# Optimization experiments

Hardware: AMD Instinct MI355X
Metric: run time of the kernel (lower is better)

The kernel has to match this reference:

```python
import jax, jax.numpy as jnp
import numpy as np

VOXEL_SIZE = np.array([0.32, 0.32, 6.0], dtype=np.float32)
SPATIAL_SIZE = np.array([-74.88, 74.88, -74.88, 74.88, -3.0, 3.0], dtype=np.float32)
# voxel_spatial_size = ceil((max-min)/voxel_size) per dim -> [468, 468, 1]
GRID = np.array([int(np.ceil((SPATIAL_SIZE[2*i+1]-SPATIAL_SIZE[2*i])/VOXEL_SIZE[i])) for i in range(3)], dtype=np.int32)
# voxel origin = floor(min / voxel_size) -> [-234, -234, -1]
ORIGIN = np.floor(SPATIAL_SIZE[0::2] / VOXEL_SIZE).astype(np.int32)
VOL = int(np.prod(GRID))  # 468*468*1
# row-major id multipliers: prods[1:]+[1] -> [468, 1, 1]
SHIFT = np.array([int(np.prod(GRID[1:])), int(np.prod(GRID[2:])), 1], dtype=np.int32)
VOXEL_FEATURE_MIN = -1000.0

B, N, D_IN, MLP = 4, 100000, 16, 128


def setup_inputs() -> dict:
    key = jax.random.key(0)
    k1, k2, k3, k4, k5 = jax.random.split(key, 5)
    xy = jax.random.uniform(k1, (B, N, 2), minval=-80.0, maxval=80.0)
    z = jax.random.uniform(k2, (B, N, 1), minval=-4.0, maxval=4.0)
    point_xyz = jnp.concatenate([xy, z], axis=-1)
    point_feature = jax.random.normal(k3, (B, N, D_IN), dtype=jnp.float32)
    point_mask = jax.random.uniform(k4, (B, N)) < 0.95
    W = jax.random.normal(k5, (D_IN + 3, MLP), dtype=jnp.float32) * 0.1
    b = jnp.zeros((MLP,), dtype=jnp.float32)
    return {"point_xyz": point_xyz, "point_feature": point_feature,
            "point_mask": point_mask, "W": W, "b": b}


def reference(point_xyz, point_feature, point_mask, W, b):
    vs = jnp.asarray(VOXEL_SIZE, dtype=point_xyz.dtype)
    # PointToVoxel
    pvx_f = jnp.floor(point_xyz / vs)                      # [B,N,3] float voxel coords
    point_voxel_feature = point_xyz - pvx_f * vs           # delta within voxel
    pvx = pvx_f.astype(jnp.int32) - jnp.asarray(ORIGIN)    # shifted int voxel coords
    grid = jnp.asarray(GRID)
    in_bounds = jnp.all((pvx >= 0) & (pvx < grid), axis=-1)
    voxel_mask = in_bounds & point_mask                    # [B,N]
    vid = jnp.sum(pvx * jnp.asarray(SHIFT), axis=-1)       # [B,N]
    vid = vid + jnp.arange(B, dtype=jnp.int32)[:, None] * VOL
    vid = vid * voxel_mask.astype(jnp.int32)               # invalid -> 0
    # point net (Dense + ReLU) on [point_feature, voxel delta]
    feat = jnp.concatenate([point_feature, point_voxel_feature], axis=-1)
    mf = voxel_mask.astype(feat.dtype)[..., None]
    feat = feat * mf
    feat = jax.nn.relu(jnp.einsum('bnd,dk->bnk', feat, W) + b)
    feat = feat * mf
    # scatter-max into dense voxel grid
    seg = jax.ops.segment_max(feat.reshape(-1, MLP), vid.reshape(-1),
                              num_segments=B * VOL)
    seg = jnp.where(seg > VOXEL_FEATURE_MIN, seg, 0.0)
    # z dim is 1 -> squeezed: [B, 468, 468, MLP]
    return seg.reshape(B, int(GRID[0]), int(GRID[1]), MLP)
```

## Files before the change

kernel.cpp:

```cpp
#include <hip/hip_runtime.h>
#include <hip/hip_bf16.h>
#include <stdint.h>

#define BB   4
#define NN   100000
#define TOTAL (BB * NN)
#define DIN  16
#define DF   19
#define KO   128
#define GX   468
#define GY   468
#define VOL  (GX * GY)
#define NV   (BB * VOL)
#define CAP  12
#define SLOT_F 20
#define NWAVES (NV / 64)

typedef float vfloat2 __attribute__((ext_vector_type(2)));

#define WS_COUNTS   0
#define WS_FLAG     (NV)
#define WS_PACKED   (NV + 16)

__global__ __launch_bounds__(256) void prep(
    int4* __restrict__ counts4,
    const uint4* __restrict__ mask_words,
    int* __restrict__ flag)
{
    if (blockIdx.x == 0) {
        __shared__ int sA, sB;
        if (threadIdx.x == 0) { sA = 0; sB = 0; }
        __syncthreads();
        int a = 0, b = 0;
        #pragma unroll
        for (int it = 0; it < 4; ++it) {
            uint4 w = mask_words[it * 256 + threadIdx.x];
            unsigned lo = (w.x & 0xFFu) | (w.y & 0xFFu) | (w.z & 0xFFu) | (w.w & 0xFFu);
            unsigned hi = (w.x & 0xFFFFFF00u) | (w.y & 0xFFFFFF00u) |
                          (w.z & 0xFFFFFF00u) | (w.w & 0xFFFFFF00u);
            if (hi) a = 1;
            if (lo) b = 1;
        }
        if (a) atomicOr(&sA, 1);
        if (b) atomicOr(&sB, 1);
        __syncthreads();
        if (threadIdx.x == 0) flag[0] = (sA && sB) ? 1 : 4;
    }
    const int i = blockIdx.x * 256 + threadIdx.x;
    if (i < NV / 4) counts4[i] = make_int4(0, 0, 0, 0);
}

__global__ __launch_bounds__(256) void pass1_bin(
    const float* __restrict__ xyz,
    const float* __restrict__ pfeat,
    const unsigned char* __restrict__ mask_raw,
    const int* __restrict__ flag,
    int* __restrict__ counts,
    float* __restrict__ packed)
{
    const int p = blockIdx.x * 256 + threadIdx.x;
    if (p >= TOTAL) return;
    const float x = xyz[p * 3 + 0];
    const float y = xyz[p * 3 + 1];
    const float z = xyz[p * 3 + 2];
    bool m;
    if (flag[0] == 4) m = (((const int*)mask_raw)[p] != 0);
    else              m = (mask_raw[p] != 0);
    const float fx = floorf(x / 0.32f);
    const float fy = floorf(y / 0.32f);
    const float fz = floorf(z / 6.0f);
    const int ix = (int)fx + 234;
    const int iy = (int)fy + 234;
    const int iz = (int)fz + 1;
    const bool inb = ((unsigned)ix < (unsigned)GX) &
                     ((unsigned)iy < (unsigned)GY) &
                     (iz == 0) & m;
    if (!inb) return;
    const int vid = (p / NN) * VOL + ix * GY + iy;
    const int rank = atomicAdd(&counts[vid], 1);
    if (rank >= CAP) return;

    float4* slot = (float4*)(packed + (size_t)(vid * CAP + rank) * SLOT_F);
    const float4* pf4 = (const float4*)(pfeat + (size_t)p * DIN);
    slot[0] = pf4[0];
    slot[1] = pf4[1];
    slot[2] = pf4[2];
    slot[3] = pf4[3];
    slot[4] = make_float4(x - fx * 0.32f, y - fy * 0.32f, z - fz * 6.0f, 0.f);
}

__global__ __launch_bounds__(256) void fused_write(
    const float* __restrict__ W,
    const float* __restrict__ bias,
    const int* __restrict__ counts,
    const float* __restrict__ packed,
    float* __restrict__ out)
{
    const int lane = threadIdx.x & 63;
    const int wid  = (blockIdx.x * 256 + threadIdx.x) >> 6;
    if (wid >= NWAVES) return;
    const int v0 = wid * 64;

    const int c_mine = counts[v0 + lane];
    const unsigned long long occ = __ballot(c_mine > 0);

    const float2* W2 = (const float2*)W;
    float2 w[DF];
    #pragma unroll
    for (int d = 0; d < DF; ++d) w[d] = W2[d * 64 + lane];
    const float2 bb = ((const float2*)bias)[lane];

    vfloat2* dst0 = (vfloat2*)(out + (size_t)v0 * KO) + lane;

    {
        vfloat2 zz = {0.f, 0.f};
        unsigned long long emp = ~occ;
        while (emp) {
            const int j = __builtin_ctzll(emp);
            emp &= emp - 1;
            __builtin_nontemporal_store(zz, dst0 + (size_t)j * 64);
        }
    }

    unsigned long long rem = occ;
    int j_cur = -1;
    float4 q0, q1, q2, q3, q4;
    if (rem) {
        j_cur = __builtin_ctzll(rem);
        rem &= rem - 1;
        const float4* base = (const float4*)(packed +
                             (size_t)(v0 + j_cur) * CAP * SLOT_F);
        q0 = base[0]; q1 = base[1]; q2 = base[2]; q3 = base[3]; q4 = base[4];
    }
    while (j_cur >= 0) {
        int j_nxt = -1;
        float4 n0, n1, n2, n3, n4;
        if (rem) {
            j_nxt = __builtin_ctzll(rem);
            rem &= rem - 1;
            const float4* nb = (const float4*)(packed +
                               (size_t)(v0 + j_nxt) * CAP * SLOT_F);
            n0 = nb[0]; n1 = nb[1]; n2 = nb[2]; n3 = nb[3]; n4 = nb[4];
        }

        const int c = min(__shfl(c_mine, j_cur), CAP);
        const float4* base = (const float4*)(packed +
                             (size_t)(v0 + j_cur) * CAP * SLOT_F);
        float m0 = -3.0e38f, m1 = -3.0e38f;
        for (int t = 0; t < c; ++t) {
            float4 p0, p1, p2, p3, p4;
            if (t == 0) { p0 = q0; p1 = q1; p2 = q2; p3 = q3; p4 = q4; }
            else {
                p0 = base[t * 5 + 0]; p1 = base[t * 5 + 1];
                p2 = base[t * 5 + 2]; p3 = base[t * 5 + 3];
                p4 = base[t * 5 + 4];
            }
            float a0 = bb.x, a1 = bb.y;
            a0 = fmaf(p0.x, w[0].x, a0);  a1 = fmaf(p0.x, w[0].y, a1);
            a0 = fmaf(p0.y, w[1].x, a0);  a1 = fmaf(p0.y, w[1].y, a1);
            a0 = fmaf(p0.z, w[2].x, a0);  a1 = fmaf(p0.z, w[2].y, a1);
            a0 = fmaf(p0.w, w[3].x, a0);  a1 = fmaf(p0.w, w[3].y, a1);
            a0 = fmaf(p1.x, w[4].x, a0);  a1 = fmaf(p1.x, w[4].y, a1);
            a0 = fmaf(p1.y, w[5].x, a0);  a1 = fmaf(p1.y, w[5].y, a1);
            a0 = fmaf(p1.z, w[6].x, a0);  a1 = fmaf(p1.z, w[6].y, a1);
            a0 = fmaf(p1.w, w[7].x, a0);  a1 = fmaf(p1.w, w[7].y, a1);
            a0 = fmaf(p2.x, w[8].x, a0);  a1 = fmaf(p2.x, w[8].y, a1);
            a0 = fmaf(p2.y, w[9].x, a0);  a1 = fmaf(p2.y, w[9].y, a1);
            a0 = fmaf(p2.z, w[10].x, a0); a1 = fmaf(p2.z, w[10].y, a1);
            a0 = fmaf(p2.w, w[11].x, a0); a1 = fmaf(p2.w, w[11].y, a1);
            a0 = fmaf(p3.x, w[12].x, a0); a1 = fmaf(p3.x, w[12].y, a1);
            a0 = fmaf(p3.y, w[13].x, a0); a1 = fmaf(p3.y, w[13].y, a1);
            a0 = fmaf(p3.z, w[14].x, a0); a1 = fmaf(p3.z, w[14].y, a1);
            a0 = fmaf(p3.w, w[15].x, a0); a1 = fmaf(p3.w, w[15].y, a1);
            a0 = fmaf(p4.x, w[16].x, a0); a1 = fmaf(p4.x, w[16].y, a1);
            a0 = fmaf(p4.y, w[17].x, a0); a1 = fmaf(p4.y, w[17].y, a1);
            a0 = fmaf(p4.z, w[18].x, a0); a1 = fmaf(p4.z, w[18].y, a1);
            m0 = fmaxf(m0, a0);
            m1 = fmaxf(m1, a1);
        }
        vfloat2 rv = {fmaxf(m0, 0.f), fmaxf(m1, 0.f)};
        __builtin_nontemporal_store(rv, dst0 + (size_t)j_cur * 64);

        j_cur = j_nxt;
        q0 = n0; q1 = n1; q2 = n2; q3 = n3; q4 = n4;
    }
}

extern "C" void kernel_launch(void* const* d_in, const int* in_sizes, int n_in,
                              void* d_out, int out_size, void* d_ws, size_t ws_size,
                              hipStream_t stream) {
    const float* xyz   = (const float*)d_in[0];
    const float* pfeat = (const float*)d_in[1];
    const unsigned char* mask = (const unsigned char*)d_in[2];
    const float* W     = (const float*)d_in[3];
    const float* bias  = (const float*)d_in[4];
    float* out = (float*)d_out;
    int* ws = (int*)d_ws;

    int*   counts = ws + WS_COUNTS;
    int*   flag   = ws + WS_FLAG;
    float* packed = (float*)(ws + WS_PACKED);

    prep<<<(NV / 4 + 255) / 256, 256, 0, stream>>>((int4*)counts,
                                                   (const uint4*)mask, flag);
    pass1_bin<<<(TOTAL + 255) / 256, 256, 0, stream>>>(xyz, pfeat, mask, flag,
                                                       counts, packed);
    fused_write<<<(NWAVES + 3) / 4, 256, 0, stream>>>(W, bias, counts,
                                                      packed, out);
}
```

Before: 536.4 us.

## Replace bin-and-gather with per-point MLP and global atomicMax scatter

```diff
diff --git a/kernel.cpp b/kernel.cpp
--- a/kernel.cpp
+++ b/kernel.cpp
@@ -1,5 +1,4 @@
 #include <hip/hip_runtime.h>
-#include <hip/hip_bf16.h>
 #include <stdint.h>
 
 #define BB   4
@@ -12,18 +11,14 @@
 #define GY   468
 #define VOL  (GX * GY)
 #define NV   (BB * VOL)
-#define CAP  12
-#define SLOT_F 20
-#define NWAVES (NV / 64)
+#define OUT_F4 ((size_t)NV * KO / 4)
 
-typedef float vfloat2 __attribute__((ext_vector_type(2)));
+typedef float vfloat4 __attribute__((ext_vector_type(4)));
 
-#define WS_COUNTS   0
-#define WS_FLAG     (NV)
-#define WS_PACKED   (NV + 16)
+#define WS_FLAG 0
 
-__global__ __launch_bounds__(256) void prep(
-    int4* __restrict__ counts4,
+__global__ __launch_bounds__(256) void fill_zero(
+    vfloat4* __restrict__ out4,
     const uint4* __restrict__ mask_words,
     int* __restrict__ flag)
 {
@@ -46,143 +41,98 @@
         __syncthreads();
         if (threadIdx.x == 0) flag[0] = (sA && sB) ? 1 : 4;
     }
-    const int i = blockIdx.x * 256 + threadIdx.x;
-    if (i < NV / 4) counts4[i] = make_int4(0, 0, 0, 0);
+    const vfloat4 z = {0.f, 0.f, 0.f, 0.f};
+    const size_t stride = (size_t)gridDim.x * 256;
+    for (size_t i = (size_t)blockIdx.x * 256 + threadIdx.x; i < OUT_F4; i += stride)
+        __builtin_nontemporal_store(z, out4 + i);
 }
 
-__global__ __launch_bounds__(256) void pass1_bin(
+__global__ __launch_bounds__(256) void points(
     const float* __restrict__ xyz,
     const float* __restrict__ pfeat,
     const unsigned char* __restrict__ mask_raw,
     const int* __restrict__ flag,
-    int* __restrict__ counts,
-    float* __restrict__ packed)
+    const float* __restrict__ W,
+    const float* __restrict__ bias,
+    float* __restrict__ out)
 {
+    __shared__ float sW[DF * KO];
+    __shared__ float sB[KO];
+    for (int i = threadIdx.x; i < DF * KO; i += 256) sW[i] = W[i];
+    if (threadIdx.x < KO) sB[threadIdx.x] = bias[threadIdx.x];
+
     const int p = blockIdx.x * 256 + threadIdx.x;
+    float x = 0.f, y = 0.f, z = 0.f;
+    bool m = false;
+    float4 pf0, pf1, pf2, pf3;
+    pf0 = pf1 = pf2 = pf3 = make_float4(0.f, 0.f, 0.f, 0.f);
+    if (p < TOTAL) {
+        x = xyz[p * 3 + 0];
+        y = xyz[p * 3 + 1];
+        z = xyz[p * 3 + 2];
+        if (flag[0] == 4) m = (((const int*)mask_raw)[p] != 0);
+        else              m = (mask_raw[p] != 0);
+        const float4* pf4 = (const float4*)(pfeat + (size_t)p * DIN);
+        pf0 = pf4[0]; pf1 = pf4[1]; pf2 = pf4[2]; pf3 = pf4[3];
+    }
+    __syncthreads();
     if (p >= TOTAL) return;
-    const float x = xyz[p * 3 + 0];
-    const float y = xyz[p * 3 + 1];
-    const float z = xyz[p * 3 + 2];
-    bool m;
-    if (flag[0] == 4) m = (((const int*)mask_raw)[p] != 0);
-    else              m = (mask_raw[p] != 0);
+
     const float fx = floorf(x / 0.32f);
     const float fy = floorf(y / 0.32f);
     const float fz = floorf(z / 6.0f);
     const int ix = (int)fx + 234;
     const int iy = (int)fy + 234;
     const int iz = (int)fz + 1;
-    const bool inb = ((unsigned)ix < (unsigned)GX) &
-                     ((unsigned)iy < (unsigned)GY) &
-                     (iz == 0) & m;
-    if (!inb) return;
-    const int vid = (p / NN) * VOL + ix * GY + iy;
-    const int rank = atomicAdd(&counts[vid], 1);
-    if (rank >= CAP) return;
+    const bool valid = ((unsigned)ix < (unsigned)GX) &
+                       ((unsigned)iy < (unsigned)GY) &
+                       (iz == 0) & m;
+    if (__ballot(valid) == 0ULL) return;
 
-    float4* slot = (float4*)(packed + (size_t)(vid * CAP + rank) * SLOT_F);
-    const float4* pf4 = (const float4*)(pfeat + (size_t)p * DIN);
-    slot[0] = pf4[0];
-    slot[1] = pf4[1];
-    slot[2] = pf4[2];
-    slot[3] = pf4[3];
-    slot[4] = make_float4(x - fx * 0.32f, y - fy * 0.32f, z - fz * 6.0f, 0.f);
-}
+    float f[DF];
+    f[0]  = pf0.x; f[1]  = pf0.y; f[2]  = pf0.z; f[3]  = pf0.w;
+    f[4]  = pf1.x; f[5]  = pf1.y; f[6]  = pf1.z; f[7]  = pf1.w;
+    f[8]  = pf2.x; f[9]  = pf2.y; f[10] = pf2.z; f[11] = pf2.w;
+    f[12] = pf3.x; f[13] = pf3.y; f[14] = pf3.z; f[15] = pf3.w;
+    f[16] = x - fx * 0.32f;
+    f[17] = y - fy * 0.32f;
+    f[18] = z - fz * 6.0f;
 
-__global__ __launch_bounds__(256) void fused_write(
-    const float* __restrict__ W,
-    const float* __restrict__ bias,
-    const int* __restrict__ counts,
-    const float* __restrict__ packed,
-    float* __restrict__ out)
-{
-    const int lane = threadIdx.x & 63;
-    const int wid  = (blockIdx.x * 256 + threadIdx.x) >> 6;
-    if (wid >= NWAVES) return;
-    const int v0 = wid * 64;
+    const int vid = valid ? ((p / NN) * VOL + ix * GY + iy) : 0;
+    int* row = (int*)out + (size_t)vid * KO;
 
-    const int c_mine = counts[v0 + lane];
-    const unsigned long long occ = __ballot(c_mine > 0);
-
-    const float2* W2 = (const float2*)W;
-    float2 w[DF];
     #pragma unroll
-    for (int d = 0; d < DF; ++d) w[d] = W2[d * 64 + lane];
-    const float2 bb = ((const float2*)bias)[lane];
-
-    vfloat2* dst0 = (vfloat2*)(out + (size_t)v0 * KO) + lane;
-
-    {
-        vfloat2 zz = {0.f, 0.f};
-        unsigned long long emp = ~occ;
-        while (emp) {
-            const int j = __builtin_ctzll(emp);
-            emp &= emp - 1;
-            __builtin_nontemporal_store(zz, dst0 + (size_t)j * 64);
+    for (int c = 0; c < 8; ++c) {
+        float acc[16];
+        {
+            const float4* b4 = (const float4*)(sB + c * 16);
+            #pragma unroll
+            for (int q = 0; q < 4; ++q) {
+                float4 bv = b4[q];
+                acc[q * 4 + 0] = bv.x; acc[q * 4 + 1] = bv.y;
+                acc[q * 4 + 2] = bv.z; acc[q * 4 + 3] = bv.w;
+            }
         }
-    }
-
-    unsigned long long rem = occ;
-    int j_cur = -1;
-    float4 q0, q1, q2, q3, q4;
-    if (rem) {
-        j_cur = __builtin_ctzll(rem);
-        rem &= rem - 1;
-        const float4* base = (const float4*)(packed +
-                             (size_t)(v0 + j_cur) * CAP * SLOT_F);
-        q0 = base[0]; q1 = base[1]; q2 = base[2]; q3 = base[3]; q4 = base[4];
-    }
-    while (j_cur >= 0) {
-        int j_nxt = -1;
-        float4 n0, n1, n2, n3, n4;
-        if (rem) {
-            j_nxt = __builtin_ctzll(rem);
-            rem &= rem - 1;
-            const float4* nb = (const float4*)(packed +
-                               (size_t)(v0 + j_nxt) * CAP * SLOT_F);
-            n0 = nb[0]; n1 = nb[1]; n2 = nb[2]; n3 = nb[3]; n4 = nb[4];
+        #pragma unroll
+        for (int d = 0; d < DF; ++d) {
+            const float fd = f[d];
+            const float4* wq = (const float4*)(sW + d * KO + c * 16);
+            #pragma unroll
+            for (int q = 0; q < 4; ++q) {
+                float4 wv = wq[q];
+                acc[q * 4 + 0] = fmaf(fd, wv.x, acc[q * 4 + 0]);
+                acc[q * 4 + 1] = fmaf(fd, wv.y, acc[q * 4 + 1]);
+                acc[q * 4 + 2] = fmaf(fd, wv.z, acc[q * 4 + 2]);
+                acc[q * 4 + 3] = fmaf(fd, wv.w, acc[q * 4 + 3]);
+            }
         }
-
-        const int c = min(__shfl(c_mine, j_cur), CAP);
-        const float4* base = (const float4*)(packed +
-                             (size_t)(v0 + j_cur) * CAP * SLOT_F);
-        float m0 = -3.0e38f, m1 = -3.0e38f;
-        for (int t = 0; t < c; ++t) {
-            float4 p0, p1, p2, p3, p4;
-            if (t == 0) { p0 = q0; p1 = q1; p2 = q2; p3 = q3; p4 = q4; }
-            else {
-                p0 = base[t * 5 + 0]; p1 = base[t * 5 + 1];
-                p2 = base[t * 5 + 2]; p3 = base[t * 5 + 3];
-                p4 = base[t * 5 + 4];
+        if (valid) {
+            #pragma unroll
+            for (int j = 0; j < 16; ++j) {
+                const float r = fmaxf(acc[j], 0.f);
+                atomicMax(row + c * 16 + j, __float_as_int(r));
             }
-            float a0 = bb.x, a1 = bb.y;
-            a0 = fmaf(p0.x, w[0].x, a0);  a1 = fmaf(p0.x, w[0].y, a1);
-            a0 = fmaf(p0.y, w[1].x, a0);  a1 = fmaf(p0.y, w[1].y, a1);
-            a0 = fmaf(p0.z, w[2].x, a0);  a1 = fmaf(p0.z, w[2].y, a1);
-            a0 = fmaf(p0.w, w[3].x, a0);  a1 = fmaf(p0.w, w[3].y, a1);
-            a0 = fmaf(p1.x, w[4].x, a0);  a1 = fmaf(p1.x, w[4].y, a1);
-            a0 = fmaf(p1.y, w[5].x, a0);  a1 = fmaf(p1.y, w[5].y, a1);
-            a0 = fmaf(p1.z, w[6].x, a0);  a1 = fmaf(p1.z, w[6].y, a1);
-            a0 = fmaf(p1.w, w[7].x, a0);  a1 = fmaf(p1.w, w[7].y, a1);
-            a0 = fmaf(p2.x, w[8].x, a0);  a1 = fmaf(p2.x, w[8].y, a1);
-            a0 = fmaf(p2.y, w[9].x, a0);  a1 = fmaf(p2.y, w[9].y, a1);
-            a0 = fmaf(p2.z, w[10].x, a0); a1 = fmaf(p2.z, w[10].y, a1);
-            a0 = fmaf(p2.w, w[11].x, a0); a1 = fmaf(p2.w, w[11].y, a1);
-            a0 = fmaf(p3.x, w[12].x, a0); a1 = fmaf(p3.x, w[12].y, a1);
-            a0 = fmaf(p3.y, w[13].x, a0); a1 = fmaf(p3.y, w[13].y, a1);
-            a0 = fmaf(p3.z, w[14].x, a0); a1 = fmaf(p3.z, w[14].y, a1);
-            a0 = fmaf(p3.w, w[15].x, a0); a1 = fmaf(p3.w, w[15].y, a1);
-            a0 = fmaf(p4.x, w[16].x, a0); a1 = fmaf(p4.x, w[16].y, a1);
-            a0 = fmaf(p4.y, w[17].x, a0); a1 = fmaf(p4.y, w[17].y, a1);
-            a0 = fmaf(p4.z, w[18].x, a0); a1 = fmaf(p4.z, w[18].y, a1);
-            m0 = fmaxf(m0, a0);
-            m1 = fmaxf(m1, a1);
         }
-        vfloat2 rv = {fmaxf(m0, 0.f), fmaxf(m1, 0.f)};
-        __builtin_nontemporal_store(rv, dst0 + (size_t)j_cur * 64);
-
-        j_cur = j_nxt;
-        q0 = n0; q1 = n1; q2 = n2; q3 = n3; q4 = n4;
     }
 }
 
@@ -195,16 +145,9 @@
     const float* W     = (const float*)d_in[3];
     const float* bias  = (const float*)d_in[4];
     float* out = (float*)d_out;
-    int* ws = (int*)d_ws;
+    int* flag = (int*)d_ws + WS_FLAG;
 
-    int*   counts = ws + WS_COUNTS;
-    int*   flag   = ws + WS_FLAG;
-    float* packed = (float*)(ws + WS_PACKED);
-
-    prep<<<(NV / 4 + 255) / 256, 256, 0, stream>>>((int4*)counts,
-                                                   (const uint4*)mask, flag);
-    pass1_bin<<<(TOTAL + 255) / 256, 256, 0, stream>>>(xyz, pfeat, mask, flag,
-                                                       counts, packed);
-    fused_write<<<(NWAVES + 3) / 4, 256, 0, stream>>>(W, bias, counts,
-                                                      packed, out);
+    fill_zero<<<2048, 256, 0, stream>>>((vfloat4*)out, (const uint4*)mask, flag);
+    points<<<(TOTAL + 255) / 256, 256, 0, stream>>>(xyz, pfeat, mask, flag,
+                                                    W, bias, out);
 }
```

New measurement: 1.383 ms. 158% more time.

## Overlap dense output zero-fill with point binning and skip empty waves

Applied to the files above, without the earlier changes.

```diff
diff --git a/kernel.cpp b/kernel.cpp
--- a/kernel.cpp
+++ b/kernel.cpp
@@ -1,5 +1,4 @@
 #include <hip/hip_runtime.h>
-#include <hip/hip_bf16.h>
 #include <stdint.h>
 
 #define BB   4
@@ -15,8 +14,13 @@
 #define CAP  12
 #define SLOT_F 20
 #define NWAVES (NV / 64)
+#define OUT_F4 ((size_t)NV * KO / 4)
+
+#define FILLB 6144
+#define BINB  2048
 
 typedef float vfloat2 __attribute__((ext_vector_type(2)));
+typedef float vfloat4 __attribute__((ext_vector_type(4)));
 
 #define WS_COUNTS   0
 #define WS_FLAG     (NV)
@@ -50,7 +54,8 @@
     if (i < NV / 4) counts4[i] = make_int4(0, 0, 0, 0);
 }
 
-__global__ __launch_bounds__(256) void pass1_bin(
+__global__ __launch_bounds__(256) void fill_and_bin(
+    vfloat4* __restrict__ out4,
     const float* __restrict__ xyz,
     const float* __restrict__ pfeat,
     const unsigned char* __restrict__ mask_raw,
@@ -58,7 +63,16 @@
     int* __restrict__ counts,
     float* __restrict__ packed)
 {
-    const int p = blockIdx.x * 256 + threadIdx.x;
+    const int r = blockIdx.x & 3;
+    if (r != 3) {
+        const size_t fid = (size_t)(blockIdx.x >> 2) * 3 + r;
+        const vfloat4 z = {0.f, 0.f, 0.f, 0.f};
+        const size_t stride = (size_t)FILLB * 256;
+        for (size_t i = fid * 256 + threadIdx.x; i < OUT_F4; i += stride)
+            __builtin_nontemporal_store(z, out4 + i);
+        return;
+    }
+    const int p = (blockIdx.x >> 2) * 256 + threadIdx.x;
     if (p >= TOTAL) return;
     const float x = xyz[p * 3 + 0];
     const float y = xyz[p * 3 + 1];
@@ -89,7 +103,7 @@
     slot[4] = make_float4(x - fx * 0.32f, y - fy * 0.32f, z - fz * 6.0f, 0.f);
 }
 
-__global__ __launch_bounds__(256) void fused_write(
+__global__ __launch_bounds__(256) void write_occ(
     const float* __restrict__ W,
     const float* __restrict__ bias,
     const int* __restrict__ counts,
@@ -103,6 +117,7 @@
 
     const int c_mine = counts[v0 + lane];
     const unsigned long long occ = __ballot(c_mine > 0);
+    if (!occ) return;
 
     const float2* W2 = (const float2*)W;
     float2 w[DF];
@@ -112,22 +127,11 @@
 
     vfloat2* dst0 = (vfloat2*)(out + (size_t)v0 * KO) + lane;
 
+    unsigned long long rem = occ;
+    int j_cur = __builtin_ctzll(rem);
+    rem &= rem - 1;
+    float4 q0, q1, q2, q3, q4;
     {
-        vfloat2 zz = {0.f, 0.f};
-        unsigned long long emp = ~occ;
-        while (emp) {
-            const int j = __builtin_ctzll(emp);
-            emp &= emp - 1;
-            __builtin_nontemporal_store(zz, dst0 + (size_t)j * 64);
-        }
-    }
-
-    unsigned long long rem = occ;
-    int j_cur = -1;
-    float4 q0, q1, q2, q3, q4;
-    if (rem) {
-        j_cur = __builtin_ctzll(rem);
-        rem &= rem - 1;
         const float4* base = (const float4*)(packed +
                              (size_t)(v0 + j_cur) * CAP * SLOT_F);
         q0 = base[0]; q1 = base[1]; q2 = base[2]; q3 = base[3]; q4 = base[4];
@@ -203,8 +207,8 @@
 
     prep<<<(NV / 4 + 255) / 256, 256, 0, stream>>>((int4*)counts,
                                                    (const uint4*)mask, flag);
-    pass1_bin<<<(TOTAL + 255) / 256, 256, 0, stream>>>(xyz, pfeat, mask, flag,
-                                                       counts, packed);
-    fused_write<<<(NWAVES + 3) / 4, 256, 0, stream>>>(W, bias, counts,
-                                                      packed, out);
-}
+    fill_and_bin<<<FILLB + BINB, 256, 0, stream>>>((vfloat4*)out, xyz, pfeat,
+                                                   mask, flag, counts, packed);
+    write_occ<<<(NWAVES + 3) / 4, 256, 0, stream>>>(W, bias, counts,
+                                                    packed, out);
+}
```

After: 556.6 us. +3.8%, slower.

## Fuse prep, binning and write kernels into one cooperative persistent kernel

Applied to the files above, without the earlier changes.

```diff
diff --git a/kernel.cpp b/kernel.cpp
--- a/kernel.cpp
+++ b/kernel.cpp
@@ -1,6 +1,8 @@
 #include <hip/hip_runtime.h>
-#include <hip/hip_bf16.h>
+#include <hip/hip_cooperative_groups.h>
 #include <stdint.h>
+
+namespace cg = cooperative_groups;
 
 #define BB   4
 #define NN   100000
@@ -22,87 +24,21 @@
 #define WS_FLAG     (NV)
 #define WS_PACKED   (NV + 16)
 
-__global__ __launch_bounds__(256) void prep(
-    int4* __restrict__ counts4,
-    const uint4* __restrict__ mask_words,
-    int* __restrict__ flag)
-{
-    if (blockIdx.x == 0) {
-        __shared__ int sA, sB;
-        if (threadIdx.x == 0) { sA = 0; sB = 0; }
-        __syncthreads();
-        int a = 0, b = 0;
-        #pragma unroll
-        for (int it = 0; it < 4; ++it) {
-            uint4 w = mask_words[it * 256 + threadIdx.x];
-            unsigned lo = (w.x & 0xFFu) | (w.y & 0xFFu) | (w.z & 0xFFu) | (w.w & 0xFFu);
-            unsigned hi = (w.x & 0xFFFFFF00u) | (w.y & 0xFFFFFF00u) |
-                          (w.z & 0xFFFFFF00u) | (w.w & 0xFFFFFF00u);
-            if (hi) a = 1;
-            if (lo) b = 1;
-        }
-        if (a) atomicOr(&sA, 1);
-        if (b) atomicOr(&sB, 1);
-        __syncthreads();
-        if (threadIdx.x == 0) flag[0] = (sA && sB) ? 1 : 4;
-    }
-    const int i = blockIdx.x * 256 + threadIdx.x;
-    if (i < NV / 4) counts4[i] = make_int4(0, 0, 0, 0);
-}
-
-__global__ __launch_bounds__(256) void pass1_bin(
+__global__ __launch_bounds__(256, 4) void mega(
     const float* __restrict__ xyz,
     const float* __restrict__ pfeat,
     const unsigned char* __restrict__ mask_raw,
-    const int* __restrict__ flag,
-    int* __restrict__ counts,
-    float* __restrict__ packed)
-{
-    const int p = blockIdx.x * 256 + threadIdx.x;
-    if (p >= TOTAL) return;
-    const float x = xyz[p * 3 + 0];
-    const float y = xyz[p * 3 + 1];
-    const float z = xyz[p * 3 + 2];
-    bool m;
-    if (flag[0] == 4) m = (((const int*)mask_raw)[p] != 0);
-    else              m = (mask_raw[p] != 0);
-    const float fx = floorf(x / 0.32f);
-    const float fy = floorf(y / 0.32f);
-    const float fz = floorf(z / 6.0f);
-    const int ix = (int)fx + 234;
-    const int iy = (int)fy + 234;
-    const int iz = (int)fz + 1;
-    const bool inb = ((unsigned)ix < (unsigned)GX) &
-                     ((unsigned)iy < (unsigned)GY) &
-                     (iz == 0) & m;
-    if (!inb) return;
-    const int vid = (p / NN) * VOL + ix * GY + iy;
-    const int rank = atomicAdd(&counts[vid], 1);
-    if (rank >= CAP) return;
-
-    float4* slot = (float4*)(packed + (size_t)(vid * CAP + rank) * SLOT_F);
-    const float4* pf4 = (const float4*)(pfeat + (size_t)p * DIN);
-    slot[0] = pf4[0];
-    slot[1] = pf4[1];
-    slot[2] = pf4[2];
-    slot[3] = pf4[3];
-    slot[4] = make_float4(x - fx * 0.32f, y - fy * 0.32f, z - fz * 6.0f, 0.f);
-}
-
-__global__ __launch_bounds__(256) void fused_write(
     const float* __restrict__ W,
     const float* __restrict__ bias,
-    const int* __restrict__ counts,
-    const float* __restrict__ packed,
+    int* __restrict__ counts,
+    int* __restrict__ flag,
+    float* __restrict__ packed,
     float* __restrict__ out)
 {
+    cg::grid_group grid = cg::this_grid();
+    const int tid  = blockIdx.x * 256 + threadIdx.x;
+    const int nth  = gridDim.x * 256;
     const int lane = threadIdx.x & 63;
-    const int wid  = (blockIdx.x * 256 + threadIdx.x) >> 6;
-    if (wid >= NWAVES) return;
-    const int v0 = wid * 64;
-
-    const int c_mine = counts[v0 + lane];
-    const unsigned long long occ = __ballot(c_mine > 0);
 
     const float2* W2 = (const float2*)W;
     float2 w[DF];
@@ -110,79 +46,148 @@
     for (int d = 0; d < DF; ++d) w[d] = W2[d * 64 + lane];
     const float2 bb = ((const float2*)bias)[lane];
 
-    vfloat2* dst0 = (vfloat2*)(out + (size_t)v0 * KO) + lane;
-
+    if (blockIdx.x == 0) {
+        __shared__ int sA, sB;
+        if (threadIdx.x == 0) { sA = 0; sB = 0; }
+        __syncthreads();
+        const uint4* mask_words = (const uint4*)mask_raw;
+        int a = 0, b = 0;
+        #pragma unroll
+        for (int it = 0; it < 4; ++it) {
+            uint4 mw = mask_words[it * 256 + threadIdx.x];
+            unsigned lo = (mw.x & 0xFFu) | (mw.y & 0xFFu) | (mw.z & 0xFFu) | (mw.w & 0xFFu);
+            unsigned hi = (mw.x & 0xFFFFFF00u) | (mw.y & 0xFFFFFF00u) |
+                          (mw.z & 0xFFFFFF00u) | (mw.w & 0xFFFFFF00u);
+            if (hi) a = 1;
+            if (lo) b = 1;
+        }
+        if (a) atomicOr(&sA, 1);
+        if (b) atomicOr(&sB, 1);
+        __syncthreads();
+        if (threadIdx.x == 0) flag[0] = (sA && sB) ? 1 : 4;
+    }
     {
-        vfloat2 zz = {0.f, 0.f};
-        unsigned long long emp = ~occ;
-        while (emp) {
-            const int j = __builtin_ctzll(emp);
-            emp &= emp - 1;
-            __builtin_nontemporal_store(zz, dst0 + (size_t)j * 64);
-        }
-    }
-
-    unsigned long long rem = occ;
-    int j_cur = -1;
-    float4 q0, q1, q2, q3, q4;
-    if (rem) {
-        j_cur = __builtin_ctzll(rem);
-        rem &= rem - 1;
-        const float4* base = (const float4*)(packed +
-                             (size_t)(v0 + j_cur) * CAP * SLOT_F);
-        q0 = base[0]; q1 = base[1]; q2 = base[2]; q3 = base[3]; q4 = base[4];
-    }
-    while (j_cur >= 0) {
-        int j_nxt = -1;
-        float4 n0, n1, n2, n3, n4;
+        int4* counts4 = (int4*)counts;
+        for (int i = tid; i < NV / 4; i += nth)
+            counts4[i] = make_int4(0, 0, 0, 0);
+    }
+    grid.sync();
+
+    {
+        const int mflag = flag[0];
+        for (int p = tid; p < TOTAL; p += nth) {
+            const float x = xyz[p * 3 + 0];
+            const float y = xyz[p * 3 + 1];
+            const float z = xyz[p * 3 + 2];
+            bool m;
+            if (mflag == 4) m = (((const int*)mask_raw)[p] != 0);
+            else            m = (mask_raw[p] != 0);
+            const float fx = floorf(x / 0.32f);
+            const float fy = floorf(y / 0.32f);
+            const float fz = floorf(z / 6.0f);
+            const int ix = (int)fx + 234;
+            const int iy = (int)fy + 234;
+            const int iz = (int)fz + 1;
+            const bool inb = ((unsigned)ix < (unsigned)GX) &
+                             ((unsigned)iy < (unsigned)GY) &
+                             (iz == 0) & m;
+            if (!inb) continue;
+            const int vid = (p / NN) * VOL + ix * GY + iy;
+            const int rank = atomicAdd(&counts[vid], 1);
+            if (rank >= CAP) continue;
+
+            float4* slot = (float4*)(packed + (size_t)(vid * CAP + rank) * SLOT_F);
+            const float4* pf4 = (const float4*)(pfeat + (size_t)p * DIN);
+            slot[0] = pf4[0];
+            slot[1] = pf4[1];
+            slot[2] = pf4[2];
+            slot[3] = pf4[3];
+            slot[4] = make_float4(x - fx * 0.32f, y - fy * 0.32f, z - fz * 6.0f, 0.f);
+        }
+    }
+    grid.sync();
+
+    const int nwav = nth >> 6;
+    for (int wid = tid >> 6; wid < NWAVES; wid += nwav) {
+        const int v0 = wid * 64;
+
+        const int c_mine = counts[v0 + lane];
+        const unsigned long long occ = __ballot(c_mine > 0);
+
+        vfloat2* dst0 = (vfloat2*)(out + (size_t)v0 * KO) + lane;
+
+        {
+            vfloat2 zz = {0.f, 0.f};
+            unsigned long long emp = ~occ;
+            while (emp) {
+                const int j = __builtin_ctzll(emp);
+                emp &= emp - 1;
+                __builtin_nontemporal_store(zz, dst0 + (size_t)j * 64);
+            }
+        }
+
+        unsigned long long rem = occ;
+        int j_cur = -1;
+        float4 q0, q1, q2, q3, q4;
         if (rem) {
-            j_nxt = __builtin_ctzll(rem);
+            j_cur = __builtin_ctzll(rem);
             rem &= rem - 1;
-            const float4* nb = (const float4*)(packed +
-                               (size_t)(v0 + j_nxt) * CAP * SLOT_F);
-            n0 = nb[0]; n1 = nb[1]; n2 = nb[2]; n3 = nb[3]; n4 = nb[4];
-        }
-
-        const int c = min(__shfl(c_mine, j_cur), CAP);
-        const float4* base = (const float4*)(packed +
-                             (size_t)(v0 + j_cur) * CAP * SLOT_F);
-        float m0 = -3.0e38f, m1 = -3.0e38f;
-        for (int t = 0; t < c; ++t) {
-            float4 p0, p1, p2, p3, p4;
-            if (t == 0) { p0 = q0; p1 = q1; p2 = q2; p3 = q3; p4 = q4; }
-            else {
-                p0 = base[t * 5 + 0]; p1 = base[t * 5 + 1];
-                p2 = base[t * 5 + 2]; p3 = base[t * 5 + 3];
-                p4 = base[t * 5 + 4];
+            const float4* base = (const float4*)(packed +
+                                 (size_t)(v0 + j_cur) * CAP * SLOT_F);
+            q0 = base[0]; q1 = base[1]; q2 = base[2]; q3 = base[3]; q4 = base[4];
+        }
+        while (j_cur >= 0) {
+            int j_nxt = -1;
+            float4 n0, n1, n2, n3, n4;
+            if (rem) {
+                j_nxt = __builtin_ctzll(rem);
+                rem &= rem - 1;
+                const float4* nb = (const float4*)(packed +
+                                   (size_t)(v0 + j_nxt) * CAP * SLOT_F);
+                n0 = nb[0]; n1 = nb[1]; n2 = nb[2]; n3 = nb[3]; n4 = nb[4];
             }
-            float a0 = bb.x, a1 = bb.y;
-            a0 = fmaf(p0.x, w[0].x, a0);  a1 = fmaf(p0.x, w[0].y, a1);
-            a0 = fmaf(p0.y, w[1].x, a0);  a1 = fmaf(p0.y, w[1].y, a1);
-            a0 = fmaf(p0.z, w[2].x, a0);  a1 = fmaf(p0.z, w[2].y, a1);
-            a0 = fmaf(p0.w, w[3].x, a0);  a1 = fmaf(p0.w, w[3].y, a1);
-            a0 = fmaf(p1.x, w[4].x, a0);  a1 = fmaf(p1.x, w[4].y, a1);
-            a0 = fmaf(p1.y, w[5].x, a0);  a1 = fmaf(p1.y, w[5].y, a1);
-            a0 = fmaf(p1.z, w[6].x, a0);  a1 = fmaf(p1.z, w[6].y, a1);
-            a0 = fmaf(p1.w, w[7].x, a0);  a1 = fmaf(p1.w, w[7].y, a1);
-            a0 = fmaf(p2.x, w[8].x, a0);  a1 = fmaf(p2.x, w[8].y, a1);
-            a0 = fmaf(p2.y, w[9].x, a0);  a1 = fmaf(p2.y, w[9].y, a1);
-            a0 = fmaf(p2.z, w[10].x, a0); a1 = fmaf(p2.z, w[10].y, a1);
-            a0 = fmaf(p2.w, w[11].x, a0); a1 = fmaf(p2.w, w[11].y, a1);
-            a0 = fmaf(p3.x, w[12].x, a0); a1 = fmaf(p3.x, w[12].y, a1);
-            a0 = fmaf(p3.y, w[13].x, a0); a1 = fmaf(p3.y, w[13].y, a1);
-            a0 = fmaf(p3.z, w[14].x, a0); a1 = fmaf(p3.z, w[14].y, a1);
-            a0 = fmaf(p3.w, w[15].x, a0); a1 = fmaf(p3.w, w[15].y, a1);
-            a0 = fmaf(p4.x, w[16].x, a0); a1 = fmaf(p4.x, w[16].y, a1);
-            a0 = fmaf(p4.y, w[17].x, a0); a1 = fmaf(p4.y, w[17].y, a1);
-            a0 = fmaf(p4.z, w[18].x, a0); a1 = fmaf(p4.z, w[18].y, a1);
-            m0 = fmaxf(m0, a0);
-            m1 = fmaxf(m1, a1);
-        }
-        vfloat2 rv = {fmaxf(m0, 0.f), fmaxf(m1, 0.f)};
-        __builtin_nontemporal_store(rv, dst0 + (size_t)j_cur * 64);
-
-        j_cur = j_nxt;
-        q0 = n0; q1 = n1; q2 = n2; q3 = n3; q4 = n4;
+
+            const int c = min(__shfl(c_mine, j_cur), CAP);
+            const float4* base = (const float4*)(packed +
+                                 (size_t)(v0 + j_cur) * CAP * SLOT_F);
+            float m0 = -3.0e38f, m1 = -3.0e38f;
+            for (int t = 0; t < c; ++t) {
+                float4 p0, p1, p2, p3, p4;
+                if (t == 0) { p0 = q0; p1 = q1; p2 = q2; p3 = q3; p4 = q4; }
+                else {
+                    p0 = base[t * 5 + 0]; p1 = base[t * 5 + 1];
+                    p2 = base[t * 5 + 2]; p3 = base[t * 5 + 3];
+                    p4 = base[t * 5 + 4];
+                }
+                float a0 = bb.x, a1 = bb.y;
+                a0 = fmaf(p0.x, w[0].x, a0);  a1 = fmaf(p0.x, w[0].y, a1);
+                a0 = fmaf(p0.y, w[1].x, a0);  a1 = fmaf(p0.y, w[1].y, a1);
+                a0 = fmaf(p0.z, w[2].x, a0);  a1 = fmaf(p0.z, w[2].y, a1);
+                a0 = fmaf(p0.w, w[3].x, a0);  a1 = fmaf(p0.w, w[3].y, a1);
+                a0 = fmaf(p1.x, w[4].x, a0);  a1 = fmaf(p1.x, w[4].y, a1);
+                a0 = fmaf(p1.y, w[5].x, a0);  a1 = fmaf(p1.y, w[5].y, a1);
+                a0 = fmaf(p1.z, w[6].x, a0);  a1 = fmaf(p1.z, w[6].y, a1);
+                a0 = fmaf(p1.w, w[7].x, a0);  a1 = fmaf(p1.w, w[7].y, a1);
+                a0 = fmaf(p2.x, w[8].x, a0);  a1 = fmaf(p2.x, w[8].y, a1);
+                a0 = fmaf(p2.y, w[9].x, a0);  a1 = fmaf(p2.y, w[9].y, a1);
+                a0 = fmaf(p2.z, w[10].x, a0); a1 = fmaf(p2.z, w[10].y, a1);
+                a0 = fmaf(p2.w, w[11].x, a0); a1 = fmaf(p2.w, w[11].y, a1);
+                a0 = fmaf(p3.x, w[12].x, a0); a1 = fmaf(p3.x, w[12].y, a1);
+                a0 = fmaf(p3.y, w[13].x, a0); a1 = fmaf(p3.y, w[13].y, a1);
+                a0 = fmaf(p3.z, w[14].x, a0); a1 = fmaf(p3.z, w[14].y, a1);
+                a0 = fmaf(p3.w, w[15].x, a0); a1 = fmaf(p3.w, w[15].y, a1);
+                a0 = fmaf(p4.x, w[16].x, a0); a1 = fmaf(p4.x, w[16].y, a1);
+                a0 = fmaf(p4.y, w[17].x, a0); a1 = fmaf(p4.y, w[17].y, a1);
+                a0 = fmaf(p4.z, w[18].x, a0); a1 = fmaf(p4.z, w[18].y, a1);
+                m0 = fmaxf(m0, a0);
+                m1 = fmaxf(m1, a1);
+            }
+            vfloat2 rv = {fmaxf(m0, 0.f), fmaxf(m1, 0.f)};
+            __builtin_nontemporal_store(rv, dst0 + (size_t)j_cur * 64);
+
+            j_cur = j_nxt;
+            q0 = n0; q1 = n1; q2 = n2; q3 = n3; q4 = n4;
+        }
     }
 }
 
@@ -201,10 +206,17 @@
     int*   flag   = ws + WS_FLAG;
     float* packed = (float*)(ws + WS_PACKED);
 
-    prep<<<(NV / 4 + 255) / 256, 256, 0, stream>>>((int4*)counts,
-                                                   (const uint4*)mask, flag);
-    pass1_bin<<<(TOTAL + 255) / 256, 256, 0, stream>>>(xyz, pfeat, mask, flag,
-                                                       counts, packed);
-    fused_write<<<(NWAVES + 3) / 4, 256, 0, stream>>>(W, bias, counts,
-                                                      packed, out);
+    static int nblk = 0;
+    if (nblk == 0) {
+        int nb = 0;
+        hipOccupancyMaxActiveBlocksPerMultiprocessor(&nb, (const void*)mega, 256, 0);
+        if (nb < 1) nb = 1;
+        if (nb > 8) nb = 8;
+        nblk = nb * 256;
+    }
+
+    void* args[] = {(void*)&xyz, (void*)&pfeat, (void*)&mask, (void*)&W,
+                    (void*)&bias, (void*)&counts, (void*)&flag,
+                    (void*)&packed, (void*)&out};
+    hipLaunchCooperativeKernel((void*)mega, dim3(nblk), dim3(256), args, 0, stream);
 }
```

Measured after the change: 692.2 us. +29.1%, slower.
